# Kernel optimization log

Hardware: AMD Instinct MI355X
Metric: run time of the kernel (lower is better)

The kernel has to match this reference:

```python
import jax, jax.numpy as jnp
import numpy as np

NUM_NODES = 10000
NODE_DIM = 128
EDGE_DIM = 128
HIDDEN_DIM = 128
OUT_DIM = 128
N_EDGES = 640000


def setup_inputs() -> dict:
    key = jax.random.key(0)
    k = jax.random.split(key, 8)
    x = jax.random.normal(k[0], (NUM_NODES, NODE_DIM), dtype=jnp.float32)
    edge_index = jax.random.randint(k[1], (2, N_EDGES), 0, NUM_NODES, dtype=jnp.int64)
    edge_attr = jax.random.normal(k[2], (N_EDGES, EDGE_DIM), dtype=jnp.float32)
    # node2edge linear: in = 2*node_dim + edge_dim
    s1 = 1.0 / np.sqrt(2 * NODE_DIM + EDGE_DIM)
    W1 = jax.random.uniform(k[3], (2 * NODE_DIM + EDGE_DIM, HIDDEN_DIM), jnp.float32, -s1, s1)
    b1 = jax.random.uniform(k[4], (HIDDEN_DIM,), jnp.float32, -s1, s1)
    # edge2node linear: in = hidden_dim + node_dim
    s2 = 1.0 / np.sqrt(HIDDEN_DIM + NODE_DIM)
    W2 = jax.random.uniform(k[5], (HIDDEN_DIM + NODE_DIM, OUT_DIM), jnp.float32, -s2, s2)
    b2 = jax.random.uniform(k[6], (OUT_DIM,), jnp.float32, -s2, s2)
    return {"x": x, "edge_index": edge_index, "edge_attr": edge_attr,
            "W1": W1, "b1": b1, "W2": W2, "b2": b2}


def reference(x, edge_index, edge_attr, W1, b1, W2, b2):
    src, dst = edge_index[0], edge_index[1]
    # Node2Edge: gather endpoints, concat with edge features, linear
    h_i = x[src]                                   # [E, node_dim]
    h_j = x[dst]                                   # [E, node_dim]
    inp_e = jnp.concatenate([h_i, h_j, edge_attr], axis=-1)  # [E, 2*nd+ed]
    h_edge = inp_e @ W1 + b1                       # [E, hidden]
    # Edge2Node: scatter-sum edge embeddings to target nodes (edge_index[1])
    agg = jax.ops.segment_sum(h_edge, dst, num_segments=NUM_NODES)  # [N, hidden]
    inp_n = jnp.concatenate([agg, x], axis=-1)     # [N, hidden+nd]
    h_node = inp_n @ W2 + b2                       # [N, out]
    return h_node
```

## Files before the change

### kernel.cpp

```cpp
#include <hip/hip_runtime.h>


#define NN 10000
#define ED 640000
#define D  128

typedef __bf16 bf16;
typedef bf16  bf16x8 __attribute__((ext_vector_type(8)));
typedef float f32x4  __attribute__((ext_vector_type(4)));

__device__ __forceinline__ bf16 f2b(float f) {
  unsigned u = __builtin_bit_cast(unsigned, f);
  u += 0x7fffu + ((u >> 16) & 1u);
  unsigned short h = (unsigned short)(u >> 16);
  return __builtin_bit_cast(bf16, h);
}

__device__ __forceinline__ bf16x8 bzero8() {
  bf16 z = __builtin_bit_cast(bf16, (unsigned short)0);
  bf16x8 v = {z, z, z, z, z, z, z, z};
  return v;
}

__global__ __launch_bounds__(256) void k_prep(const float* __restrict__ x,
                                              const float* __restrict__ W1,
                                              const float* __restrict__ W2,
                                              bf16* __restrict__ xb,
                                              bf16* __restrict__ W1p,
                                              bf16* __restrict__ W1bp,
                                              bf16* __restrict__ W2p,
                                              int* __restrict__ counts) {
  int id = blockIdx.x * 256 + threadIdx.x;
  if (id < 160000) {
    int i = id * 8;
    f32x4 a = *(const f32x4*)(x + i);
    f32x4 b = *(const f32x4*)(x + i + 4);
    bf16x8 h;
    h[0]=f2b(a[0]); h[1]=f2b(a[1]); h[2]=f2b(a[2]); h[3]=f2b(a[3]);
    h[4]=f2b(b[0]); h[5]=f2b(b[1]); h[6]=f2b(b[2]); h[7]=f2b(b[3]);
    *(bf16x8*)(xb + i) = h;
  } else if (id < 170000) {
    counts[id - 160000] = 0;
  } else if (id < 174096) {
    int o8 = id - 170000;
    int kb = o8 >> 9, rem = o8 & 511, t = rem >> 6, L = rem & 63;
    int col = t * 16 + (L & 15);
    int k0  = kb * 32 + (L >> 4) * 8;
    int row0 = (kb < 4) ? k0 : (k0 + 128);
    bf16x8 h;
    #pragma unroll
    for (int j = 0; j < 8; j++) h[j] = f2b(W1[(row0 + j) * D + col]);
    *(bf16x8*)(W1p + o8 * 8) = h;
  } else if (id < 176144) {
    int o8 = id - 174096;
    int kb = o8 >> 9, rem = o8 & 511, t = rem >> 6, L = rem & 63;
    int col = t * 16 + (L & 15);
    int row0 = 128 + kb * 32 + (L >> 4) * 8;
    bf16x8 h;
    #pragma unroll
    for (int j = 0; j < 8; j++) h[j] = f2b(W1[(row0 + j) * D + col]);
    *(bf16x8*)(W1bp + o8 * 8) = h;
  } else if (id < 180240) {
    int o8 = id - 176144;
    int kb = o8 >> 9, rem = o8 & 511, t = rem >> 6, L = rem & 63;
    int col = t * 16 + (L & 15);
    int row0 = kb * 32 + (L >> 4) * 8;
    bf16x8 h;
    #pragma unroll
    for (int j = 0; j < 8; j++) h[j] = f2b(W2[(row0 + j) * D + col]);
    *(bf16x8*)(W2p + o8 * 8) = h;
  }
}

__global__ __launch_bounds__(256) void k_hist(const int* __restrict__ dst,
                                              int* __restrict__ counts) {
  int e = blockIdx.x * 256 + threadIdx.x;
  if (e < ED) atomicAdd(&counts[dst[e]], 1);
}

__global__ __launch_bounds__(256) void k_scan(const int* __restrict__ counts,
                                              int* __restrict__ row_ptr,
                                              int* __restrict__ fill_ptr) {
  __shared__ int part[256];
  int tid = threadIdx.x;
  const int CH = 40;
  int base = tid * CH;
  int sum = 0;
  for (int i = 0; i < CH; i++) { int idx = base + i; if (idx < NN) sum += counts[idx]; }
  part[tid] = sum;
  __syncthreads();
  for (int off = 1; off < 256; off <<= 1) {
    int v = (tid >= off) ? part[tid - off] : 0;
    __syncthreads();
    part[tid] += v;
    __syncthreads();
  }
  int run = part[tid] - sum;
  for (int i = 0; i < CH; i++) {
    int idx = base + i;
    if (idx < NN) { row_ptr[idx] = run; fill_ptr[idx] = run; run += counts[idx]; }
  }
  if (tid == 255) row_ptr[NN] = part[255];
}

__global__ __launch_bounds__(256) void k_fill(const int* __restrict__ src,
                                              const int* __restrict__ dst,
                                              int* __restrict__ fill_ptr,
                                              int* __restrict__ csr_eid,
                                              int* __restrict__ csr_src) {
  int e = blockIdx.x * 256 + threadIdx.x;
  if (e < ED) {
    int d = dst[e];
    int pos = atomicAdd(&fill_ptr[d], 1);
    csr_eid[pos] = e;
    csr_src[pos] = src[e];
  }
}

#define K5_GRID 2048
__global__ __launch_bounds__(256) void k_edge(const bf16*  __restrict__ xb,
                                              const float* __restrict__ ea,
                                              const bf16*  __restrict__ W1p,
                                              const float* __restrict__ b1,
                                              const int*   __restrict__ row_ptr,
                                              const int*   __restrict__ csr_eid,
                                              const int*   __restrict__ csr_src,
                                              float* __restrict__ agg) {
  __shared__ __align__(16) bf16 As[16][264];
  int tid  = threadIdx.x;
  int wave = tid >> 6, lane = tid & 63, quad = lane >> 4, l16 = lane & 15;
  int srow = tid >> 4, scol = tid & 15;

  bf16x8 B[8][2];
  #pragma unroll
  for (int kb = 0; kb < 8; kb++)
    #pragma unroll
    for (int tt = 0; tt < 2; tt++)
      B[kb][tt] = *(const bf16x8*)(W1p + ((kb * 8 + (wave * 2 + tt)) * 64 + lane) * 8);

  for (int v = blockIdx.x; v < NN; v += K5_GRID) {
    int e0 = row_ptr[v], e1 = row_ptr[v + 1];
    int cnt = e1 - e0;
    f32x4 acc0 = {0.f, 0.f, 0.f, 0.f};
    f32x4 acc1 = {0.f, 0.f, 0.f, 0.f};
    int ntile = (cnt + 15) >> 4;
    for (int t = 0; t < ntile; t++) {
      int e = e0 + t * 16 + srow;
      if (e < e1) {
        int eid = csr_eid[e];
        int sid = csr_src[e];
        *(bf16x8*)&As[srow][scol * 8] = *(const bf16x8*)(xb + sid * D + scol * 8);
        const float* ep = ea + (size_t)eid * D + scol * 8;
        f32x4 f0 = *(const f32x4*)ep;
        f32x4 f1 = *(const f32x4*)(ep + 4);
        bf16x8 h;
        h[0]=f2b(f0[0]); h[1]=f2b(f0[1]); h[2]=f2b(f0[2]); h[3]=f2b(f0[3]);
        h[4]=f2b(f1[0]); h[5]=f2b(f1[1]); h[6]=f2b(f1[2]); h[7]=f2b(f1[3]);
        *(bf16x8*)&As[srow][128 + scol * 8] = h;
      } else {
        bf16x8 z = bzero8();
        *(bf16x8*)&As[srow][scol * 8] = z;
        *(bf16x8*)&As[srow][128 + scol * 8] = z;
      }
      __syncthreads();
      #pragma unroll
      for (int kb = 0; kb < 8; kb++) {
        bf16x8 a = *(const bf16x8*)&As[l16][kb * 32 + quad * 8];
        acc0 = __builtin_amdgcn_mfma_f32_16x16x32_bf16(a, B[kb][0], acc0, 0, 0, 0);
        acc1 = __builtin_amdgcn_mfma_f32_16x16x32_bf16(a, B[kb][1], acc1, 0, 0, 0);
      }
      __syncthreads();
    }
    float s0 = acc0[0] + acc0[1] + acc0[2] + acc0[3];
    float s1 = acc1[0] + acc1[1] + acc1[2] + acc1[3];
    s0 += __shfl_xor(s0, 16, 64);  s0 += __shfl_xor(s0, 32, 64);
    s1 += __shfl_xor(s1, 16, 64);  s1 += __shfl_xor(s1, 32, 64);
    int cbase = wave * 32;
    if (lane < 16) {
      int c = cbase + lane;
      agg[v * D + c] = s0 + (float)cnt * b1[c];
    } else if (lane < 32) {
      int c = cbase + 16 + (lane & 15);
      agg[v * D + c] = s1 + (float)cnt * b1[c];
    }
  }
}

__global__ __launch_bounds__(256) void k_selfterm(const bf16* __restrict__ xb,
                                                  const bf16* __restrict__ W1bp,
                                                  const int*  __restrict__ row_ptr,
                                                  float* __restrict__ agg) {
  __shared__ __align__(16) bf16 As[64][136];
  int tid  = threadIdx.x;
  int wave = tid >> 6, lane = tid & 63, quad = lane >> 4, l16 = lane & 15;
  int n0 = blockIdx.x * 64;

  bf16x8 B[4][2];
  #pragma unroll
  for (int kb = 0; kb < 4; kb++)
    #pragma unroll
    for (int tt = 0; tt < 2; tt++)
      B[kb][tt] = *(const bf16x8*)(W1bp + ((kb * 8 + (wave * 2 + tt)) * 64 + lane) * 8);

  #pragma unroll
  for (int i = 0; i < 4; i++) {
    int g = tid + 256 * i;
    int row = g >> 4, c8 = g & 15;
    int v = n0 + row;
    bf16x8 h = (v < NN) ? *(const bf16x8*)(xb + v * D + c8 * 8) : bzero8();
    *(bf16x8*)&As[row][c8 * 8] = h;
  }
  __syncthreads();

  f32x4 acc[4][2];
  #pragma unroll
  for (int mt = 0; mt < 4; mt++)
    #pragma unroll
    for (int tt = 0; tt < 2; tt++) acc[mt][tt] = (f32x4){0.f, 0.f, 0.f, 0.f};

  #pragma unroll
  for (int kb = 0; kb < 4; kb++)
    #pragma unroll
    for (int mt = 0; mt < 4; mt++) {
      bf16x8 a = *(const bf16x8*)&As[mt * 16 + l16][kb * 32 + quad * 8];
      acc[mt][0] = __builtin_amdgcn_mfma_f32_16x16x32_bf16(a, B[kb][0], acc[mt][0], 0, 0, 0);
      acc[mt][1] = __builtin_amdgcn_mfma_f32_16x16x32_bf16(a, B[kb][1], acc[mt][1], 0, 0, 0);
    }

  #pragma unroll
  for (int mt = 0; mt < 4; mt++)
    #pragma unroll
    for (int tt = 0; tt < 2; tt++)
      #pragma unroll
      for (int r = 0; r < 4; r++) {
        int v = n0 + mt * 16 + quad * 4 + r;
        if (v < NN) {
          int c = wave * 32 + tt * 16 + l16;
          float cntf = (float)(row_ptr[v + 1] - row_ptr[v]);
          agg[v * D + c] += cntf * acc[mt][tt][r];
        }
      }
}

__global__ __launch_bounds__(256) void k_node(const float* __restrict__ agg,
                                              const bf16*  __restrict__ xb,
                                              const bf16*  __restrict__ W2p,
                                              const float* __restrict__ b2,
                                              float* __restrict__ out) {
  __shared__ __align__(16) bf16 As[64][264];
  int tid  = threadIdx.x;
  int wave = tid >> 6, lane = tid & 63, quad = lane >> 4, l16 = lane & 15;
  int n0 = blockIdx.x * 64;

  bf16x8 B[8][2];
  #pragma unroll
  for (int kb = 0; kb < 8; kb++)
    #pragma unroll
    for (int tt = 0; tt < 2; tt++)
      B[kb][tt] = *(const bf16x8*)(W2p + ((kb * 8 + (wave * 2 + tt)) * 64 + lane) * 8);

  #pragma unroll
  for (int i = 0; i < 8; i++) {
    int g = tid + 256 * i;
    int row = g >> 5, c8 = g & 31;
    int v = n0 + row;
    if (c8 < 16) {
      bf16x8 h;
      if (v < NN) {
        const float* ap = agg + v * D + c8 * 8;
        f32x4 f0 = *(const f32x4*)ap;
        f32x4 f1 = *(const f32x4*)(ap + 4);
        h[0]=f2b(f0[0]); h[1]=f2b(f0[1]); h[2]=f2b(f0[2]); h[3]=f2b(f0[3]);
        h[4]=f2b(f1[0]); h[5]=f2b(f1[1]); h[6]=f2b(f1[2]); h[7]=f2b(f1[3]);
      } else h = bzero8();
      *(bf16x8*)&As[row][c8 * 8] = h;
    } else {
      int c8b = c8 - 16;
      bf16x8 h = (v < NN) ? *(const bf16x8*)(xb + v * D + c8b * 8) : bzero8();
      *(bf16x8*)&As[row][128 + c8b * 8] = h;
    }
  }
  __syncthreads();

  f32x4 acc[4][2];
  #pragma unroll
  for (int mt = 0; mt < 4; mt++)
    #pragma unroll
    for (int tt = 0; tt < 2; tt++) acc[mt][tt] = (f32x4){0.f, 0.f, 0.f, 0.f};

  #pragma unroll
  for (int kb = 0; kb < 8; kb++)
    #pragma unroll
    for (int mt = 0; mt < 4; mt++) {
      bf16x8 a = *(const bf16x8*)&As[mt * 16 + l16][kb * 32 + quad * 8];
      acc[mt][0] = __builtin_amdgcn_mfma_f32_16x16x32_bf16(a, B[kb][0], acc[mt][0], 0, 0, 0);
      acc[mt][1] = __builtin_amdgcn_mfma_f32_16x16x32_bf16(a, B[kb][1], acc[mt][1], 0, 0, 0);
    }

  #pragma unroll
  for (int mt = 0; mt < 4; mt++)
    #pragma unroll
    for (int tt = 0; tt < 2; tt++)
      #pragma unroll
      for (int r = 0; r < 4; r++) {
        int v = n0 + mt * 16 + quad * 4 + r;
        if (v < NN) {
          int c = wave * 32 + tt * 16 + l16;
          out[v * D + c] = acc[mt][tt][r] + b2[c];
        }
      }
}

extern "C" void kernel_launch(void* const* d_in, const int* in_sizes, int n_in,
                              void* d_out, int out_size, void* d_ws, size_t ws_size,
                              hipStream_t stream) {
  const float* x  = (const float*)d_in[0];
  const int*   ei = (const int*)  d_in[1];
  const float* ea = (const float*)d_in[2];
  const float* W1 = (const float*)d_in[3];
  const float* b1 = (const float*)d_in[4];
  const float* W2 = (const float*)d_in[5];
  const float* b2 = (const float*)d_in[6];
  float* out = (float*)d_out;

  char* ws = (char*)d_ws;
  size_t off = 0;
  auto alloc = [&](size_t bytes) -> void* {
    void* p = ws + off;
    off += (bytes + 255) & ~(size_t)255;
    return p;
  };
  bf16* xb       = (bf16*)alloc((size_t)NN * D * 2);
  bf16* W1p      = (bf16*)alloc(32768 * 2);
  bf16* W1bp     = (bf16*)alloc(16384 * 2);
  bf16* W2p      = (bf16*)alloc(32768 * 2);
  float* agg     = (float*)alloc((size_t)NN * D * 4);
  int* counts    = (int*)alloc(NN * 4);
  int* row_ptr   = (int*)alloc((NN + 1) * 4);
  int* fill_ptr  = (int*)alloc(NN * 4);
  int* csr_eid   = (int*)alloc((size_t)ED * 4);
  int* csr_src   = (int*)alloc((size_t)ED * 4);
  (void)ws_size; (void)in_sizes; (void)n_in; (void)out_size;

  const int* src = ei;
  const int* dst = ei + ED;

  k_prep<<<705, 256, 0, stream>>>(x, W1, W2, xb, W1p, W1bp, W2p, counts);
  k_hist<<<(ED + 255) / 256, 256, 0, stream>>>(dst, counts);
  k_scan<<<1, 256, 0, stream>>>(counts, row_ptr, fill_ptr);
  k_fill<<<(ED + 255) / 256, 256, 0, stream>>>(src, dst, fill_ptr, csr_eid, csr_src);
  k_edge<<<K5_GRID, 256, 0, stream>>>(xb, ea, W1p, b1, row_ptr, csr_eid, csr_src, agg);
  k_selfterm<<<(NN + 63) / 64, 256, 0, stream>>>(xb, W1bp, row_ptr, agg);
  k_node<<<(NN + 63) / 64, 256, 0, stream>>>(agg, xb, W2p, b2, out);
}
```

Baseline: 615.4 us.

## Aggregate edge inputs before the linear layer, then apply fused node GEMMs

Because the first linear layer is linear, the per-destination sums of gathered source features and edge attributes are computed first in a wave-per-node reduction kernel. A single fused node kernel then applies W1 (source sum, count-scaled self term, edge-attr sum) and W2 back to back in LDS. This replaces the per-edge MFMA tile loop, the separate self-term kernel and the fp32 agg round trip. The CSR is also packed as int2. It trades per-edge GEMM work for fp32 gather-sum work plus two extra N×D fp32 buffers, and the rounding behaviour changes because the summation happens before conversion to bf16.

```diff
diff --git a/kernel.cpp b/kernel.cpp
--- a/kernel.cpp
+++ b/kernel.cpp
@@ -27,7 +27,6 @@
                                               const float* __restrict__ W2,
                                               bf16* __restrict__ xb,
                                               bf16* __restrict__ W1p,
-                                              bf16* __restrict__ W1bp,
                                               bf16* __restrict__ W2p,
                                               int* __restrict__ counts) {
   int id = blockIdx.x * 256 + threadIdx.x;
@@ -41,29 +40,19 @@
     *(bf16x8*)(xb + i) = h;
   } else if (id < 170000) {
     counts[id - 160000] = 0;
-  } else if (id < 174096) {
+  } else if (id < 176144) {
     int o8 = id - 170000;
     int kb = o8 >> 9, rem = o8 & 511, t = rem >> 6, L = rem & 63;
-    int col = t * 16 + (L & 15);
-    int k0  = kb * 32 + (L >> 4) * 8;
-    int row0 = (kb < 4) ? k0 : (k0 + 128);
+    int col  = t * 16 + (L & 15);
+    int row0 = kb * 32 + (L >> 4) * 8;
     bf16x8 h;
     #pragma unroll
     for (int j = 0; j < 8; j++) h[j] = f2b(W1[(row0 + j) * D + col]);
     *(bf16x8*)(W1p + o8 * 8) = h;
-  } else if (id < 176144) {
-    int o8 = id - 174096;
-    int kb = o8 >> 9, rem = o8 & 511, t = rem >> 6, L = rem & 63;
-    int col = t * 16 + (L & 15);
-    int row0 = 128 + kb * 32 + (L >> 4) * 8;
-    bf16x8 h;
-    #pragma unroll
-    for (int j = 0; j < 8; j++) h[j] = f2b(W1[(row0 + j) * D + col]);
-    *(bf16x8*)(W1bp + o8 * 8) = h;
   } else if (id < 180240) {
     int o8 = id - 176144;
     int kb = o8 >> 9, rem = o8 & 511, t = rem >> 6, L = rem & 63;
-    int col = t * 16 + (L & 15);
+    int col  = t * 16 + (L & 15);
     int row0 = kb * 32 + (L >> 4) * 8;
     bf16x8 h;
     #pragma unroll
@@ -106,109 +95,104 @@
 __global__ __launch_bounds__(256) void k_fill(const int* __restrict__ src,
                                               const int* __restrict__ dst,
                                               int* __restrict__ fill_ptr,
-                                              int* __restrict__ csr_eid,
-                                              int* __restrict__ csr_src) {
+                                              int2* __restrict__ csr) {
   int e = blockIdx.x * 256 + threadIdx.x;
   if (e < ED) {
     int d = dst[e];
     int pos = atomicAdd(&fill_ptr[d], 1);
-    csr_eid[pos] = e;
-    csr_src[pos] = src[e];
-  }
-}
-
-#define K5_GRID 2048
-__global__ __launch_bounds__(256) void k_edge(const bf16*  __restrict__ xb,
-                                              const float* __restrict__ ea,
-                                              const bf16*  __restrict__ W1p,
-                                              const float* __restrict__ b1,
-                                              const int*   __restrict__ row_ptr,
-                                              const int*   __restrict__ csr_eid,
-                                              const int*   __restrict__ csr_src,
-                                              float* __restrict__ agg) {
-  __shared__ __align__(16) bf16 As[16][264];
-  int tid  = threadIdx.x;
-  int wave = tid >> 6, lane = tid & 63, quad = lane >> 4, l16 = lane & 15;
-  int srow = tid >> 4, scol = tid & 15;
-
-  bf16x8 B[8][2];
-  #pragma unroll
-  for (int kb = 0; kb < 8; kb++)
-    #pragma unroll
-    for (int tt = 0; tt < 2; tt++)
-      B[kb][tt] = *(const bf16x8*)(W1p + ((kb * 8 + (wave * 2 + tt)) * 64 + lane) * 8);
-
-  for (int v = blockIdx.x; v < NN; v += K5_GRID) {
-    int e0 = row_ptr[v], e1 = row_ptr[v + 1];
-    int cnt = e1 - e0;
-    f32x4 acc0 = {0.f, 0.f, 0.f, 0.f};
-    f32x4 acc1 = {0.f, 0.f, 0.f, 0.f};
-    int ntile = (cnt + 15) >> 4;
-    for (int t = 0; t < ntile; t++) {
-      int e = e0 + t * 16 + srow;
-      if (e < e1) {
-        int eid = csr_eid[e];
-        int sid = csr_src[e];
-        *(bf16x8*)&As[srow][scol * 8] = *(const bf16x8*)(xb + sid * D + scol * 8);
-        const float* ep = ea + (size_t)eid * D + scol * 8;
-        f32x4 f0 = *(const f32x4*)ep;
-        f32x4 f1 = *(const f32x4*)(ep + 4);
-        bf16x8 h;
-        h[0]=f2b(f0[0]); h[1]=f2b(f0[1]); h[2]=f2b(f0[2]); h[3]=f2b(f0[3]);
-        h[4]=f2b(f1[0]); h[5]=f2b(f1[1]); h[6]=f2b(f1[2]); h[7]=f2b(f1[3]);
-        *(bf16x8*)&As[srow][128 + scol * 8] = h;
-      } else {
-        bf16x8 z = bzero8();
-        *(bf16x8*)&As[srow][scol * 8] = z;
-        *(bf16x8*)&As[srow][128 + scol * 8] = z;
-      }
-      __syncthreads();
-      #pragma unroll
-      for (int kb = 0; kb < 8; kb++) {
-        bf16x8 a = *(const bf16x8*)&As[l16][kb * 32 + quad * 8];
-        acc0 = __builtin_amdgcn_mfma_f32_16x16x32_bf16(a, B[kb][0], acc0, 0, 0, 0);
-        acc1 = __builtin_amdgcn_mfma_f32_16x16x32_bf16(a, B[kb][1], acc1, 0, 0, 0);
-      }
-      __syncthreads();
-    }
-    float s0 = acc0[0] + acc0[1] + acc0[2] + acc0[3];
-    float s1 = acc1[0] + acc1[1] + acc1[2] + acc1[3];
-    s0 += __shfl_xor(s0, 16, 64);  s0 += __shfl_xor(s0, 32, 64);
-    s1 += __shfl_xor(s1, 16, 64);  s1 += __shfl_xor(s1, 32, 64);
-    int cbase = wave * 32;
-    if (lane < 16) {
-      int c = cbase + lane;
-      agg[v * D + c] = s0 + (float)cnt * b1[c];
-    } else if (lane < 32) {
-      int c = cbase + 16 + (lane & 15);
-      agg[v * D + c] = s1 + (float)cnt * b1[c];
-    }
-  }
-}
-
-__global__ __launch_bounds__(256) void k_selfterm(const bf16* __restrict__ xb,
-                                                  const bf16* __restrict__ W1bp,
-                                                  const int*  __restrict__ row_ptr,
-                                                  float* __restrict__ agg) {
-  __shared__ __align__(16) bf16 As[64][136];
+    csr[pos] = make_int2(e, src[e]);
+  }
+}
+
+__global__ __launch_bounds__(256) void k_sum(const bf16*  __restrict__ xb,
+                                             const float* __restrict__ ea,
+                                             const int*   __restrict__ row_ptr,
+                                             const int2*  __restrict__ csr,
+                                             float* __restrict__ sx,
+                                             float* __restrict__ sea) {
+  int gwave = (blockIdx.x * 256 + threadIdx.x) >> 6;
+  if (gwave >= NN) return;
+  int lane = threadIdx.x & 63;
+  int g = lane >> 4, l = lane & 15;
+  int e0 = row_ptr[gwave], e1 = row_ptr[gwave + 1];
+
+  f32x4 ax0 = {0.f,0.f,0.f,0.f}, ax1 = {0.f,0.f,0.f,0.f};
+  f32x4 ae0 = {0.f,0.f,0.f,0.f}, ae1 = {0.f,0.f,0.f,0.f};
+
+  #pragma unroll 2
+  for (int e = e0 + g; e < e1; e += 4) {
+    int2 es = csr[e];
+    bf16x8 hx = *(const bf16x8*)(xb + (size_t)es.y * D + l * 8);
+    const float* ep = ea + (size_t)es.x * D + l * 8;
+    f32x4 f0 = *(const f32x4*)ep;
+    f32x4 f1 = *(const f32x4*)(ep + 4);
+    ax0[0] += (float)hx[0]; ax0[1] += (float)hx[1];
+    ax0[2] += (float)hx[2]; ax0[3] += (float)hx[3];
+    ax1[0] += (float)hx[4]; ax1[1] += (float)hx[5];
+    ax1[2] += (float)hx[6]; ax1[3] += (float)hx[7];
+    ae0 += f0;
+    ae1 += f1;
+  }
+  #pragma unroll
+  for (int i = 0; i < 4; i++) {
+    ax0[i] += __shfl_xor(ax0[i], 16, 64); ax0[i] += __shfl_xor(ax0[i], 32, 64);
+    ax1[i] += __shfl_xor(ax1[i], 16, 64); ax1[i] += __shfl_xor(ax1[i], 32, 64);
+    ae0[i] += __shfl_xor(ae0[i], 16, 64); ae0[i] += __shfl_xor(ae0[i], 32, 64);
+    ae1[i] += __shfl_xor(ae1[i], 16, 64); ae1[i] += __shfl_xor(ae1[i], 32, 64);
+  }
+  if (lane < 16) {
+    float* px = sx  + (size_t)gwave * D + l * 8;
+    float* pe = sea + (size_t)gwave * D + l * 8;
+    *(f32x4*)px       = ax0;
+    *(f32x4*)(px + 4) = ax1;
+    *(f32x4*)pe       = ae0;
+    *(f32x4*)(pe + 4) = ae1;
+  }
+}
+
+__global__ __launch_bounds__(256) void k_out(const float* __restrict__ sx,
+                                             const float* __restrict__ sea,
+                                             const bf16*  __restrict__ xb,
+                                             const bf16*  __restrict__ W1p,
+                                             const bf16*  __restrict__ W2p,
+                                             const float* __restrict__ b1,
+                                             const float* __restrict__ b2,
+                                             const int*   __restrict__ row_ptr,
+                                             float* __restrict__ out) {
+  __shared__ __align__(16) bf16 lds[64 * 392];
   int tid  = threadIdx.x;
   int wave = tid >> 6, lane = tid & 63, quad = lane >> 4, l16 = lane & 15;
   int n0 = blockIdx.x * 64;
 
-  bf16x8 B[4][2];
-  #pragma unroll
-  for (int kb = 0; kb < 4; kb++)
-    #pragma unroll
-    for (int tt = 0; tt < 2; tt++)
-      B[kb][tt] = *(const bf16x8*)(W1bp + ((kb * 8 + (wave * 2 + tt)) * 64 + lane) * 8);
-
   #pragma unroll
   for (int i = 0; i < 4; i++) {
-    int g = tid + 256 * i;
-    int row = g >> 4, c8 = g & 15;
-    int v = n0 + row;
-    bf16x8 h = (v < NN) ? *(const bf16x8*)(xb + v * D + c8 * 8) : bzero8();
-    *(bf16x8*)&As[row][c8 * 8] = h;
+    int m = (tid >> 4) + 16 * i;
+    int v = n0 + m;
+    int cl = tid & 15;
+    float cntf = (v < NN) ? (float)(row_ptr[v + 1] - row_ptr[v]) : 0.f;
+    #pragma unroll
+    for (int j = 0; j < 3; j++) {
+      int c = cl + 16 * j;
+      bf16x8 h;
+      if (v < NN) {
+        if (j == 0) {
+          const float* p = sx + (size_t)v * D + cl * 8;
+          f32x4 f0 = *(const f32x4*)p, f1 = *(const f32x4*)(p + 4);
+          h[0]=f2b(f0[0]); h[1]=f2b(f0[1]); h[2]=f2b(f0[2]); h[3]=f2b(f0[3]);
+          h[4]=f2b(f1[0]); h[5]=f2b(f1[1]); h[6]=f2b(f1[2]); h[7]=f2b(f1[3]);
+        } else if (j == 1) {
+          bf16x8 hx = *(const bf16x8*)(xb + (size_t)v * D + cl * 8);
+          #pragma unroll
+          for (int k = 0; k < 8; k++) h[k] = f2b((float)hx[k] * cntf);
+        } else {
+          const float* p = sea + (size_t)v * D + cl * 8;
+          f32x4 f0 = *(const f32x4*)p, f1 = *(const f32x4*)(p + 4);
+          h[0]=f2b(f0[0]); h[1]=f2b(f0[1]); h[2]=f2b(f0[2]); h[3]=f2b(f0[3]);
+          h[4]=f2b(f1[0]); h[5]=f2b(f1[1]); h[6]=f2b(f1[2]); h[7]=f2b(f1[3]);
+        }
+      } else h = bzero8();
+      *(bf16x8*)&lds[m * 392 + c * 8] = h;
+    }
   }
   __syncthreads();
 
@@ -219,96 +203,72 @@
     for (int tt = 0; tt < 2; tt++) acc[mt][tt] = (f32x4){0.f, 0.f, 0.f, 0.f};
 
   #pragma unroll
-  for (int kb = 0; kb < 4; kb++)
+  for (int kb = 0; kb < 12; kb++) {
+    bf16x8 B0 = *(const bf16x8*)(W1p + ((kb * 8 + wave * 2 + 0) * 64 + lane) * 8);
+    bf16x8 B1 = *(const bf16x8*)(W1p + ((kb * 8 + wave * 2 + 1) * 64 + lane) * 8);
     #pragma unroll
     for (int mt = 0; mt < 4; mt++) {
-      bf16x8 a = *(const bf16x8*)&As[mt * 16 + l16][kb * 32 + quad * 8];
-      acc[mt][0] = __builtin_amdgcn_mfma_f32_16x16x32_bf16(a, B[kb][0], acc[mt][0], 0, 0, 0);
-      acc[mt][1] = __builtin_amdgcn_mfma_f32_16x16x32_bf16(a, B[kb][1], acc[mt][1], 0, 0, 0);
+      bf16x8 a = *(const bf16x8*)&lds[(mt * 16 + l16) * 392 + kb * 32 + quad * 8];
+      acc[mt][0] = __builtin_amdgcn_mfma_f32_16x16x32_bf16(a, B0, acc[mt][0], 0, 0, 0);
+      acc[mt][1] = __builtin_amdgcn_mfma_f32_16x16x32_bf16(a, B1, acc[mt][1], 0, 0, 0);
     }
-
+  }
+  __syncthreads();
+
+  #pragma unroll
+  for (int tt = 0; tt < 2; tt++) {
+    int col = wave * 32 + tt * 16 + l16;
+    float bb = b1[col];
+    #pragma unroll
+    for (int mt = 0; mt < 4; mt++)
+      #pragma unroll
+      for (int r = 0; r < 4; r++) {
+        int m = mt * 16 + quad * 4 + r;
+        int v = n0 + m;
+        float cntf = (v < NN) ? (float)(row_ptr[v + 1] - row_ptr[v]) : 0.f;
+        lds[m * 264 + col] = f2b(acc[mt][tt][r] + cntf * bb);
+      }
+  }
+  #pragma unroll
+  for (int i = 0; i < 4; i++) {
+    int m = (tid >> 4) + 16 * i;
+    int c = tid & 15;
+    int v = n0 + m;
+    bf16x8 h = (v < NN) ? *(const bf16x8*)(xb + (size_t)v * D + c * 8) : bzero8();
+    *(bf16x8*)&lds[m * 264 + 128 + c * 8] = h;
+  }
+  __syncthreads();
+
+  f32x4 acc2[4][2];
   #pragma unroll
   for (int mt = 0; mt < 4; mt++)
     #pragma unroll
-    for (int tt = 0; tt < 2; tt++)
+    for (int tt = 0; tt < 2; tt++) acc2[mt][tt] = (f32x4){0.f, 0.f, 0.f, 0.f};
+
+  #pragma unroll
+  for (int kb = 0; kb < 8; kb++) {
+    bf16x8 B0 = *(const bf16x8*)(W2p + ((kb * 8 + wave * 2 + 0) * 64 + lane) * 8);
+    bf16x8 B1 = *(const bf16x8*)(W2p + ((kb * 8 + wave * 2 + 1) * 64 + lane) * 8);
+    #pragma unroll
+    for (int mt = 0; mt < 4; mt++) {
+      bf16x8 a = *(const bf16x8*)&lds[(mt * 16 + l16) * 264 + kb * 32 + quad * 8];
+      acc2[mt][0] = __builtin_amdgcn_mfma_f32_16x16x32_bf16(a, B0, acc2[mt][0], 0, 0, 0);
+      acc2[mt][1] = __builtin_amdgcn_mfma_f32_16x16x32_bf16(a, B1, acc2[mt][1], 0, 0, 0);
+    }
+  }
+
+  #pragma unroll
+  for (int tt = 0; tt < 2; tt++) {
+    int col = wave * 32 + tt * 16 + l16;
+    float bb = b2[col];
+    #pragma unroll
+    for (int mt = 0; mt < 4; mt++)
       #pragma unroll
       for (int r = 0; r < 4; r++) {
         int v = n0 + mt * 16 + quad * 4 + r;
-        if (v < NN) {
-          int c = wave * 32 + tt * 16 + l16;
-          float cntf = (float)(row_ptr[v + 1] - row_ptr[v]);
-          agg[v * D + c] += cntf * acc[mt][tt][r];
-        }
+        if (v < NN) out[(size_t)v * D + col] = acc2[mt][tt][r] + bb;
       }
-}
-
-__global__ __launch_bounds__(256) void k_node(const float* __restrict__ agg,
-                                              const bf16*  __restrict__ xb,
-                                              const bf16*  __restrict__ W2p,
-                                              const float* __restrict__ b2,
-                                              float* __restrict__ out) {
-  __shared__ __align__(16) bf16 As[64][264];
-  int tid  = threadIdx.x;
-  int wave = tid >> 6, lane = tid & 63, quad = lane >> 4, l16 = lane & 15;
-  int n0 = blockIdx.x * 64;
-
-  bf16x8 B[8][2];
-  #pragma unroll
-  for (int kb = 0; kb < 8; kb++)
-    #pragma unroll
-    for (int tt = 0; tt < 2; tt++)
-      B[kb][tt] = *(const bf16x8*)(W2p + ((kb * 8 + (wave * 2 + tt)) * 64 + lane) * 8);
-
-  #pragma unroll
-  for (int i = 0; i < 8; i++) {
-    int g = tid + 256 * i;
-    int row = g >> 5, c8 = g & 31;
-    int v = n0 + row;
-    if (c8 < 16) {
-      bf16x8 h;
-      if (v < NN) {
-        const float* ap = agg + v * D + c8 * 8;
-        f32x4 f0 = *(const f32x4*)ap;
-        f32x4 f1 = *(const f32x4*)(ap + 4);
-        h[0]=f2b(f0[0]); h[1]=f2b(f0[1]); h[2]=f2b(f0[2]); h[3]=f2b(f0[3]);
-        h[4]=f2b(f1[0]); h[5]=f2b(f1[1]); h[6]=f2b(f1[2]); h[7]=f2b(f1[3]);
-      } else h = bzero8();
-      *(bf16x8*)&As[row][c8 * 8] = h;
-    } else {
-      int c8b = c8 - 16;
-      bf16x8 h = (v < NN) ? *(const bf16x8*)(xb + v * D + c8b * 8) : bzero8();
-      *(bf16x8*)&As[row][128 + c8b * 8] = h;
-    }
-  }
-  __syncthreads();
-
-  f32x4 acc[4][2];
-  #pragma unroll
-  for (int mt = 0; mt < 4; mt++)
-    #pragma unroll
-    for (int tt = 0; tt < 2; tt++) acc[mt][tt] = (f32x4){0.f, 0.f, 0.f, 0.f};
-
-  #pragma unroll
-  for (int kb = 0; kb < 8; kb++)
-    #pragma unroll
-    for (int mt = 0; mt < 4; mt++) {
-      bf16x8 a = *(const bf16x8*)&As[mt * 16 + l16][kb * 32 + quad * 8];
-      acc[mt][0] = __builtin_amdgcn_mfma_f32_16x16x32_bf16(a, B[kb][0], acc[mt][0], 0, 0, 0);
-      acc[mt][1] = __builtin_amdgcn_mfma_f32_16x16x32_bf16(a, B[kb][1], acc[mt][1], 0, 0, 0);
-    }
-
-  #pragma unroll
-  for (int mt = 0; mt < 4; mt++)
-    #pragma unroll
-    for (int tt = 0; tt < 2; tt++)
-      #pragma unroll
-      for (int r = 0; r < 4; r++) {
-        int v = n0 + mt * 16 + quad * 4 + r;
-        if (v < NN) {
-          int c = wave * 32 + tt * 16 + l16;
-          out[v * D + c] = acc[mt][tt][r] + b2[c];
-        }
-      }
+  }
 }
 
 extern "C" void kernel_launch(void* const* d_in, const int* in_sizes, int n_in,
@@ -330,26 +290,24 @@
     off += (bytes + 255) & ~(size_t)255;
     return p;
   };
-  bf16* xb       = (bf16*)alloc((size_t)NN * D * 2);
-  bf16* W1p      = (bf16*)alloc(32768 * 2);
-  bf16* W1bp     = (bf16*)alloc(16384 * 2);
-  bf16* W2p      = (bf16*)alloc(32768 * 2);
-  float* agg     = (float*)alloc((size_t)NN * D * 4);
-  int* counts    = (int*)alloc(NN * 4);
-  int* row_ptr   = (int*)alloc((NN + 1) * 4);
-  int* fill_ptr  = (int*)alloc(NN * 4);
-  int* csr_eid   = (int*)alloc((size_t)ED * 4);
-  int* csr_src   = (int*)alloc((size_t)ED * 4);
+  bf16*  xb      = (bf16*)alloc((size_t)NN * D * 2);
+  bf16*  W1p     = (bf16*)alloc(49152 * 2);
+  bf16*  W2p     = (bf16*)alloc(32768 * 2);
+  float* sx      = (float*)alloc((size_t)NN * D * 4);
+  float* sea     = (float*)alloc((size_t)NN * D * 4);
+  int*   counts  = (int*)alloc(NN * 4);
+  int*   row_ptr = (int*)alloc((NN + 1) * 4);
+  int*   fill_ptr= (int*)alloc(NN * 4);
+  int2*  csr     = (int2*)alloc((size_t)ED * 8);
   (void)ws_size; (void)in_sizes; (void)n_in; (void)out_size;
 
   const int* src = ei;
   const int* dst = ei + ED;
 
-  k_prep<<<705, 256, 0, stream>>>(x, W1, W2, xb, W1p, W1bp, W2p, counts);
+  k_prep<<<705, 256, 0, stream>>>(x, W1, W2, xb, W1p, W2p, counts);
   k_hist<<<(ED + 255) / 256, 256, 0, stream>>>(dst, counts);
   k_scan<<<1, 256, 0, stream>>>(counts, row_ptr, fill_ptr);
-  k_fill<<<(ED + 255) / 256, 256, 0, stream>>>(src, dst, fill_ptr, csr_eid, csr_src);
-  k_edge<<<K5_GRID, 256, 0, stream>>>(xb, ea, W1p, b1, row_ptr, csr_eid, csr_src, agg);
-  k_selfterm<<<(NN + 63) / 64, 256, 0, stream>>>(xb, W1bp, row_ptr, agg);
-  k_node<<<(NN + 63) / 64, 256, 0, stream>>>(agg, xb, W2p, b2, out);
-}
+  k_fill<<<(ED + 255) / 256, 256, 0, stream>>>(src, dst, fill_ptr, csr);
+  k_sum<<<2500, 256, 0, stream>>>(xb, ea, row_ptr, csr, sx, sea);
+  k_out<<<157, 256, 0, stream>>>(sx, sea, xb, W1p, W2p, b1, b2, row_ptr, out);
+}
```

Measured after the change: 585.9 us. 4.8% less time.
